# Optimization experiments

Hardware: AMD Instinct MI355X
Metric: run time of the kernel (lower is better)

## Reference

```python
import jax, jax.numpy as jnp
import numpy as np

B, T, V, D, H, HS, FF, L = 4, 1024, 32000, 1024, 16, 64, 4096, 8
STD = 0.02

def _ln(x, g, b, eps=1e-5):
    m = x.mean(-1, keepdims=True)
    v = ((x - m) ** 2).mean(-1, keepdims=True)
    return (x - m) / jnp.sqrt(v + eps) * g + b

def setup_inputs() -> dict:
    key = jax.random.key(0)
    ks = jax.random.split(key, 16)
    n = lambda k, shp: jax.random.normal(k, shp, dtype=jnp.float32) * STD
    inp = {
        "idx": jax.random.randint(ks[0], (B, T), 0, V),
        "tok_emb": n(ks[1], (V, D)),
        "pos_emb": n(ks[2], (T, D)),
        # per-layer stacked attention weights; [D, H, HS] per layer (no bias)
        "Wq": n(ks[3], (L, D, H, HS)),
        "Wk": n(ks[4], (L, D, H, HS)),
        "Wv": n(ks[5], (L, D, H, HS)),
        "Wp": n(ks[6], (L, H * HS, D)),
        "bp": jnp.zeros((L, D), jnp.float32),
        "ln1_g": jnp.ones((L, D), jnp.float32),
        "ln1_b": jnp.zeros((L, D), jnp.float32),
        "ln2_g": jnp.ones((L, D), jnp.float32),
        "ln2_b": jnp.zeros((L, D), jnp.float32),
        "W1": n(ks[7], (L, D, FF)),
        "b1": jnp.zeros((L, FF), jnp.float32),
        "W2": n(ks[8], (L, FF, D)),
        "b2": jnp.zeros((L, D), jnp.float32),
        "lnf_g": jnp.ones((D,), jnp.float32),
        "lnf_b": jnp.zeros((D,), jnp.float32),
        "Wlm": n(ks[9], (D, V)),
        "blm": jnp.zeros((V,), jnp.float32),
    }
    return inp

def reference(idx, tok_emb, pos_emb, Wq, Wk, Wv, Wp, bp, ln1_g, ln1_b,
              ln2_g, ln2_b, W1, b1, W2, b2, lnf_g, lnf_b, Wlm, blm):
    Bb, Tt = idx.shape
    x = tok_emb[idx] + pos_emb[:Tt]                      # [B,T,D]
    causal = jnp.tril(jnp.ones((Tt, Tt), bool))          # tril mask
    for l in range(L):
        xn = _ln(x, ln1_g[l], ln1_b[l])
        q = jnp.einsum('btd,dhk->bhtk', xn, Wq[l])
        k = jnp.einsum('btd,dhk->bhtk', xn, Wk[l])
        v = jnp.einsum('btd,dhk->bhtk', xn, Wv[l])
        w = jnp.einsum('bhtk,bhsk->bhts', q, k) * (HS ** -0.5)
        w = jnp.where(causal, w, -jnp.inf)
        w = jax.nn.softmax(w, axis=-1)
        o = jnp.einsum('bhts,bhsk->bhtk', w, v)
        o = o.transpose(0, 2, 1, 3).reshape(Bb, Tt, H * HS)  # concat heads
        x = x + o @ Wp[l] + bp[l]
        xn = _ln(x, ln2_g[l], ln2_b[l])
        x = x + jax.nn.relu(xn @ W1[l] + b1[l]) @ W2[l] + b2[l]
    x = _ln(x, lnf_g, lnf_b)
    logits = x @ Wlm + blm                               # [B,T,V]
    return logits
```

## Files before the change

### kernel.cpp

```cpp
#include <hip/hip_runtime.h>
#include <cstdint>

typedef __attribute__((ext_vector_type(4))) float f32x4;
typedef __attribute__((ext_vector_type(8))) short s16x8;
typedef __attribute__((ext_vector_type(4))) short s16x4;
typedef unsigned short u16;
typedef unsigned int u32;
typedef __attribute__((address_space(1))) void gas_void;
typedef __attribute__((address_space(3))) void las_void;

#define B_ 4
#define T_ 1024
#define V_ 32000
#define D_ 1024
#define H_ 16
#define HS_ 64
#define FF_ 4096
#define L_ 8
#define BT_ (B_ * T_)

__device__ __forceinline__ float bf2f(u16 h) { return __uint_as_float(((u32)h) << 16); }
__device__ __forceinline__ u16 f2bf(float f) {
  u32 u = __float_as_uint(f);
  u += 0x7fffu + ((u >> 16) & 1u);
  return (u16)(u >> 16);
}

__device__ __forceinline__ void gld16(const void* g, void* l) {
  __builtin_amdgcn_global_load_lds((gas_void*)(uintptr_t)g,
                                   (las_void*)(u32)(uintptr_t)l, 16, 0, 0);
}


template <int EPI>
__global__ __launch_bounds__(512, 2) void gemm256(
    const u16* __restrict__ A, const u16* __restrict__ Bt,
    const float* __restrict__ bias, float* Cf, u16* Cb,
    int M, int N, int K, int nrowb) {
  __shared__ u16 lds[2][2][2][8192];
  const int tid = threadIdx.x;
  const int lane = tid & 63;
  const int lr = lane & 15, hi = lane >> 4;
  const int wid = tid >> 6;
  const int wm128 = (wid >> 2) << 7;
  const int wn64 = (wid & 3) << 6;
  const int logical = ((int)blockIdx.x & 7) * ((int)gridDim.x >> 3) + ((int)blockIdx.x >> 3);
  const int row0 = (logical % nrowb) << 8;
  const int col0 = (logical / nrowb) << 8;
  const int NT = K >> 6;
  const int srow = tid >> 2;
  const int schunk = tid & 3;
  const int xo = ((hi + (lr >> 1)) & 3) << 4;

  f32x4 acc[32];
#pragma unroll
  for (int i = 0; i < 32; ++i) acc[i] = f32x4{0.f, 0.f, 0.f, 0.f};
  s16x8 bfr[4];

#define VMW(N) asm volatile("s_waitcnt vmcnt(" #N ")" ::: "memory")

#define STG(DB, DK, OP, KT)                                                    \
  {                                                                            \
    const u16* sp_ = (OP) ? Bt : A;                                            \
    const int base_ = (OP) ? col0 : row0;                                      \
    const int c0_ = ((KT) << 6) + ((DK) << 5);                                 \
    _Pragma("unroll")                                                          \
    for (int sh_ = 0; sh_ < 2; ++sh_) {                                        \
      const int rr_ = (sh_ << 7) + srow;                                       \
      const int ko_ = ((schunk - (rr_ >> 1)) & 3) << 3;                        \
      gld16(sp_ + (size_t)(base_ + rr_) * K + c0_ + ko_,                       \
            (char*)&lds[DB][DK][OP][0] + (sh_ << 13) + (wid << 10));           \
    }                                                                          \
  }

#define PHASE(BUF, MH, KS, LOADB, STG_STMT, VM_STMT)                           \
  {                                                                            \
    __builtin_amdgcn_sched_barrier(0);                                         \
    const char* As_ = (const char*)&lds[BUF][KS][0][0];                        \
    const char* Bs_ = (const char*)&lds[BUF][KS][1][0];                        \
    const int ra_ = wm128 + ((MH) << 6) + lr;                                  \
    s16x8 af_[4];                                                              \
    _Pragma("unroll")                                                          \
    for (int q_ = 0; q_ < 4; ++q_)                                             \
      af_[q_] = *(const s16x8*)(As_ + ((ra_ + (q_ << 4)) << 6) + xo);          \
    if (LOADB) {                                                               \
      _Pragma("unroll")                                                        \
      for (int q_ = 0; q_ < 4; ++q_)                                           \
        bfr[q_] = *(const s16x8*)(Bs_ + ((wn64 + lr + (q_ << 4)) << 6) + xo);  \
    }                                                                          \
    STG_STMT;                                                                  \
    __builtin_amdgcn_sched_barrier(0);                                         \
    __builtin_amdgcn_s_barrier();                                              \
    asm volatile("s_waitcnt lgkmcnt(0)" ::: "memory");                         \
    __builtin_amdgcn_sched_barrier(0);                                         \
    __builtin_amdgcn_s_setprio(1);                                             \
    _Pragma("unroll")                                                          \
    for (int mi_ = 0; mi_ < 4; ++mi_) {                                        \
      _Pragma("unroll")                                                        \
      for (int nj_ = 0; nj_ < 4; ++nj_)                                        \
        acc[((MH)*4 + mi_) * 4 + nj_] = __builtin_amdgcn_mfma_f32_16x16x32_bf16( \
            af_[mi_], bfr[nj_], acc[((MH)*4 + mi_) * 4 + nj_], 0, 0, 0);       \
    }                                                                          \
    __builtin_amdgcn_s_setprio(0);                                             \
    __builtin_amdgcn_sched_barrier(0);                                         \
    VM_STMT;                                                                   \
    __builtin_amdgcn_s_barrier();                                              \
  }

  STG(0, 0, 0, 0)
  STG(0, 0, 1, 0)
  STG(0, 1, 0, 0)
  STG(0, 1, 1, 0)
  STG(1, 0, 0, 1)
  STG(1, 0, 1, 1)
  VMW(8);
  __builtin_amdgcn_s_barrier();

  const int NI = NT >> 1;
  for (int it = 0; it < NI - 1; ++it) {
    const int t1 = 2 * it + 1, t2 = 2 * it + 2, t3 = 2 * it + 3;
    PHASE(0, 0, 0, 1, STG(1, 1, 0, t1), )
    PHASE(0, 1, 0, 0, STG(1, 1, 1, t1), VMW(6))
    PHASE(0, 0, 1, 1, STG(0, 0, 0, t2), )
    PHASE(0, 1, 1, 0, STG(0, 0, 1, t2), VMW(6))
    PHASE(1, 0, 0, 1, STG(0, 1, 0, t2), )
    PHASE(1, 1, 0, 0, STG(0, 1, 1, t2), VMW(6))
    PHASE(1, 0, 1, 1, STG(1, 0, 0, t3), )
    PHASE(1, 1, 1, 0, STG(1, 0, 1, t3), VMW(6))
  }
  {
    PHASE(0, 0, 0, 1, STG(1, 1, 0, NT - 1), )
    PHASE(0, 1, 0, 0, STG(1, 1, 1, NT - 1), VMW(8))
    PHASE(0, 0, 1, 1, (void)0, )
    PHASE(0, 1, 1, 0, (void)0, VMW(4))
    PHASE(1, 0, 0, 1, (void)0, )
    PHASE(1, 1, 0, 0, (void)0, VMW(0))
    PHASE(1, 0, 1, 1, (void)0, )
    PHASE(1, 1, 1, 0, (void)0, )
  }
#undef PHASE
#undef STG
#undef VMW

  const int gr0 = row0 + wm128;
  const int gc0 = col0 + wn64;
#pragma unroll
  for (int nj = 0; nj < 4; ++nj) {
    const int col = gc0 + (nj << 4) + lr;
    const float bv = (EPI != 0) ? bias[col] : 0.f;
#pragma unroll
    for (int mi = 0; mi < 8; ++mi) {
#pragma unroll
      for (int rg = 0; rg < 4; ++rg) {
        const int row = gr0 + (mi << 4) + (hi << 2) + rg;
        const size_t off = (size_t)row * N + col;
        float val = acc[mi * 4 + nj][rg] + bv;
        if constexpr (EPI == 2) val = fmaxf(val, 0.f);
        if constexpr (EPI == 0 || EPI == 2) Cb[off] = f2bf(val);
        else Cf[off] = val;
      }
    }
  }
}

template <int EPI>
__global__ __launch_bounds__(256) void gemm_bt(
    const u16* __restrict__ A, const u16* __restrict__ Bt,
    const float* __restrict__ bias, float* Cf, u16* Cb,
    int M, int N, int K) {
  __shared__ u16 lds[2][2][4096];
  const int tid = threadIdx.x;
  const int lane = tid & 63;
  const int lr = lane & 15, hi = lane >> 4;
  const int wid = tid >> 6;
  const int wm = wid >> 1, wn = wid & 1;
  const int row0 = blockIdx.y << 7, col0 = blockIdx.x << 7;
  const int NT = K >> 5;
  const int wbase = (tid & ~63) << 4;
  const int xo = ((hi + (lr >> 1)) & 3) << 4;

  f32x4 acc[4][4];
#pragma unroll
  for (int i = 0; i < 4; ++i)
#pragma unroll
    for (int j = 0; j < 4; ++j) acc[i][j] = f32x4{0.f, 0.f, 0.f, 0.f};

  auto stage = [&](int buf, int kt) {
#pragma unroll
    for (int c = 0; c < 2; ++c) {
      const int o = (c << 12) + (tid << 4);
      const int r = o >> 6;
      const int ko = ((((o >> 4) & 3) - (r >> 1)) & 3) << 3;
      gld16(A + (size_t)(row0 + r) * K + (kt << 5) + ko,
            (char*)&lds[buf][0][0] + (c << 12) + wbase);
      gld16(Bt + (size_t)(col0 + r) * K + (kt << 5) + ko,
            (char*)&lds[buf][1][0] + (c << 12) + wbase);
    }
  };

  stage(0, 0);
  __syncthreads();
  int cur = 0;
  for (int kt = 0; kt < NT; ++kt) {
    if (kt + 1 < NT) stage(cur ^ 1, kt + 1);
    const char* As = (const char*)&lds[cur][0][0];
    const char* Bs = (const char*)&lds[cur][1][0];
    s16x8 af[4], bfr[4];
#pragma unroll
    for (int i = 0; i < 4; ++i) {
      const int ra = (wm << 6) + (i << 4) + lr;
      af[i] = *(const s16x8*)(As + (ra << 6) + xo);
      const int rb = (wn << 6) + (i << 4) + lr;
      bfr[i] = *(const s16x8*)(Bs + (rb << 6) + xo);
    }
#pragma unroll
    for (int i = 0; i < 4; ++i)
#pragma unroll
      for (int j = 0; j < 4; ++j)
        acc[i][j] =
            __builtin_amdgcn_mfma_f32_16x16x32_bf16(af[i], bfr[j], acc[i][j], 0, 0, 0);
    __syncthreads();
    cur ^= 1;
  }

  const int gr = row0 + (wm << 6);
  const int gc = col0 + (wn << 6);
#pragma unroll
  for (int j = 0; j < 4; ++j) {
    const int col = gc + (j << 4) + lr;
    const float bv = (EPI != 0) ? bias[col] : 0.f;
#pragma unroll
    for (int i = 0; i < 4; ++i) {
#pragma unroll
      for (int rg = 0; rg < 4; ++rg) {
        const int row = gr + (i << 4) + (hi << 2) + rg;
        const size_t off = (size_t)row * N + col;
        float val = acc[i][j][rg] + bv;
        if constexpr (EPI == 1) val += Cf[off];
        if constexpr (EPI == 2) val = fmaxf(val, 0.f);
        if constexpr (EPI == 0 || EPI == 2) Cb[off] = f2bf(val);
        else Cf[off] = val;
      }
    }
  }
}

__global__ __launch_bounds__(256) void ln_kernel(const float* __restrict__ x,
                                                 const float* __restrict__ gw,
                                                 const float* __restrict__ bw,
                                                 u16* __restrict__ out) {
  const int r = blockIdx.x, tid = threadIdx.x;
  const int lane = tid & 63, wid = tid >> 6;
  __shared__ float red[8];
  f32x4 v = *(const f32x4*)(x + ((size_t)r << 10) + (tid << 2));
  float s = v[0] + v[1] + v[2] + v[3];
  float q = v[0] * v[0] + v[1] * v[1] + v[2] * v[2] + v[3] * v[3];
#pragma unroll
  for (int off = 32; off; off >>= 1) {
    s += __shfl_down(s, off);
    q += __shfl_down(q, off);
  }
  if (lane == 0) {
    red[wid] = s;
    red[4 + wid] = q;
  }
  __syncthreads();
  const float mean = (red[0] + red[1] + red[2] + red[3]) * (1.f / 1024.f);
  const float var = (red[4] + red[5] + red[6] + red[7]) * (1.f / 1024.f) - mean * mean;
  const float rstd = rsqrtf(var + 1e-5f);
  f32x4 g4 = *(const f32x4*)(gw + (tid << 2));
  f32x4 b4 = *(const f32x4*)(bw + (tid << 2));
  u16* op = out + ((size_t)r << 10) + (tid << 2);
#pragma unroll
  for (int j = 0; j < 4; ++j) op[j] = f2bf((v[j] - mean) * rstd * g4[j] + b4[j]);
}

__global__ __launch_bounds__(256) void embed_kernel(const int* __restrict__ idx,
                                                    const float* __restrict__ tok,
                                                    const float* __restrict__ pos,
                                                    float* __restrict__ x) {
  const int r = blockIdx.x, tid = threadIdx.x;
  const int t = r & (T_ - 1);
  const int tk = idx[r];
  f32x4 a = *(const f32x4*)(tok + ((size_t)tk << 10) + (tid << 2));
  f32x4 p = *(const f32x4*)(pos + ((size_t)t << 10) + (tid << 2));
  *(f32x4*)(x + ((size_t)r << 10) + (tid << 2)) = a + p;
}

__global__ __launch_bounds__(256) void tconv_kernel(const float* __restrict__ src,
                                                    u16* __restrict__ dst, int K, int N) {
  __shared__ float tile[32][33];
  const int tx = threadIdx.x & 31, ty = threadIdx.x >> 5;
  const int n0 = blockIdx.x << 5, k0 = blockIdx.y << 5;
#pragma unroll
  for (int i = 0; i < 32; i += 8)
    tile[ty + i][tx] = src[(size_t)(k0 + ty + i) * N + n0 + tx];
  __syncthreads();
#pragma unroll
  for (int i = 0; i < 32; i += 8)
    dst[(size_t)(n0 + ty + i) * K + k0 + tx] = f2bf(tile[tx][ty + i]);
}

__global__ __launch_bounds__(256) void fattn_kernel(const u16* __restrict__ qkv,
                                                    u16* __restrict__ o) {
  const int qt = blockIdx.x, h = blockIdx.y, b = blockIdx.z;
  const int tid = threadIdx.x;
  const int lane = tid & 63;
  const int lr = lane & 15, hi = lane >> 4;
  const int w = tid >> 6;
  __shared__ alignas(16) u16 Kl[2][4096];
  __shared__ alignas(16) u16 Vt[2][4096];

  const size_t bT = (size_t)(b * T_);
  const int q_row = (qt << 6) + (w << 4) + lr;
  const size_t qbase = (bT + q_row) * 3072 + (h << 6);
  s16x8 aq[2];
  aq[0] = *(const s16x8*)(qkv + qbase + hi * 8);
  aq[1] = *(const s16x8*)(qkv + qbase + 32 + hi * 8);

  f32x4 ofr[4];
#pragma unroll
  for (int j = 0; j < 4; ++j) ofr[j] = f32x4{0.f, 0.f, 0.f, 0.f};
  float mrun = -1e30f, lsum = 0.f;

  uint4 vr0, vr1;

#define STAGEK(BUF, KT)                                                        \
  {                                                                            \
    _Pragma("unroll")                                                          \
    for (int sh_ = 0; sh_ < 2; ++sh_) {                                        \
      const int ob_ = (sh_ << 12) + (tid << 4);                                \
      const int r_ = ob_ >> 7;                                                 \
      const int il_ = (ob_ & 127) ^ ((r_ & 7) << 4);                           \
      gld16(qkv + (bT + ((KT) << 6) + r_) * 3072 + 1024 + (h << 6) + (il_ >> 1), \
            (char*)&Kl[BUF][0] + (sh_ << 12) + ((tid & 192) << 4));            \
    }                                                                          \
  }
#define LOADV(KT)                                                              \
  {                                                                            \
    const u16* vs_ =                                                           \
        qkv + (bT + ((KT) << 6) + lane) * 3072 + 2048 + (h << 6) + (w << 4);   \
    vr0 = *(const uint4*)vs_;                                                  \
    vr1 = *(const uint4*)(vs_ + 8);                                            \
  }
#define WRITEV(BUF)                                                            \
  {                                                                            \
    const u16* p0_ = (const u16*)&vr0;                                         \
    const u16* p1_ = (const u16*)&vr1;                                         \
    _Pragma("unroll")                                                          \
    for (int j_ = 0; j_ < 8; ++j_) {                                           \
      const int sw_ = lane ^ (j_ << 3);                                        \
      Vt[BUF][(((w << 4) + j_) << 6) + sw_] = p0_[j_];                         \
      Vt[BUF][(((w << 4) + 8 + j_) << 6) + sw_] = p1_[j_];                     \
    }                                                                          \
  }

  STAGEK(0, 0)
  LOADV(0)
  asm volatile("s_waitcnt vmcnt(0)" ::: "memory");
  WRITEV(0)
  asm volatile("s_waitcnt lgkmcnt(0)" ::: "memory");
  __builtin_amdgcn_sched_barrier(0);
  __builtin_amdgcn_s_barrier();

  int cur = 0;
  for (int kt = 0; kt <= qt; ++kt) {
    if (kt < qt) {
      STAGEK(cur ^ 1, kt + 1)
      LOADV(kt + 1)
    }

    f32x4 s[4];
#pragma unroll
    for (int j = 0; j < 4; ++j) s[j] = f32x4{0.f, 0.f, 0.f, 0.f};
    __builtin_amdgcn_s_setprio(1);
#pragma unroll
    for (int kk = 0; kk < 2; ++kk)
#pragma unroll
      for (int j = 0; j < 4; ++j) {
        const int rb = (j << 4) + lr;
        const s16x8 bk = *(const s16x8*)((const char*)&Kl[cur][0] + (rb << 7) +
                                         ((((kk << 2) + hi) ^ (rb & 7)) << 4));
        s[j] = __builtin_amdgcn_mfma_f32_16x16x32_bf16(bk, aq[kk], s[j], 0, 0, 0);
      }
    __builtin_amdgcn_s_setprio(0);

    if (kt == qt) {
      const int qr = (w << 4) + lr;
#pragma unroll
      for (int j = 0; j < 4; ++j)
#pragma unroll
        for (int rg = 0; rg < 4; ++rg) {
          const int kvr = (j << 4) + (hi << 2) + rg;
          s[j][rg] = (kvr > qr) ? -1e30f : s[j][rg] * 0.125f;
        }
    } else {
#pragma unroll
      for (int j = 0; j < 4; ++j) s[j] = s[j] * 0.125f;
    }

    float mx = -1e30f;
#pragma unroll
    for (int j = 0; j < 4; ++j)
#pragma unroll
      for (int rg = 0; rg < 4; ++rg) mx = fmaxf(mx, s[j][rg]);
    mx = fmaxf(mx, __shfl_xor(mx, 16));
    mx = fmaxf(mx, __shfl_xor(mx, 32));
    const float mn = fmaxf(mrun, mx);
    const float sc = __expf(mrun - mn);
    mrun = mn;
    float rs = 0.f;
#pragma unroll
    for (int j = 0; j < 4; ++j)
#pragma unroll
      for (int rg = 0; rg < 4; ++rg) {
        const float e = __expf(s[j][rg] - mn);
        s[j][rg] = e;
        rs += e;
      }
    rs += __shfl_xor(rs, 16);
    rs += __shfl_xor(rs, 32);
    lsum = lsum * sc + rs;
    float scO[4];
#pragma unroll
    for (int rg = 0; rg < 4; ++rg) scO[rg] = __shfl(sc, (hi << 2) + rg);
#pragma unroll
    for (int j2 = 0; j2 < 4; ++j2)
#pragma unroll
      for (int rg = 0; rg < 4; ++rg) ofr[j2][rg] *= scO[rg];

    s16x8 pb[2];
#pragma unroll
    for (int kk = 0; kk < 2; ++kk)
#pragma unroll
      for (int i = 0; i < 4; ++i) {
        pb[kk][i] = (short)f2bf(s[2 * kk][i]);
        pb[kk][4 + i] = (short)f2bf(s[2 * kk + 1][i]);
      }

    __builtin_amdgcn_s_setprio(1);
#pragma unroll
    for (int kk = 0; kk < 2; ++kk)
#pragma unroll
      for (int j2 = 0; j2 < 4; ++j2) {
        const int drow = (j2 << 4) + lr;
        const int swz = (drow & 7) << 3;
        const int base = drow << 6;
        const s16x4 lo = *(const s16x4*)&Vt[cur][base + (((kk << 5) + (hi << 2)) ^ swz)];
        const s16x4 hv = *(const s16x4*)&Vt[cur][base + (((kk << 5) + 16 + (hi << 2)) ^ swz)];
        const s16x8 vb = __builtin_shufflevector(lo, hv, 0, 1, 2, 3, 4, 5, 6, 7);
        ofr[j2] = __builtin_amdgcn_mfma_f32_16x16x32_bf16(pb[kk], vb, ofr[j2], 0, 0, 0);
      }
    __builtin_amdgcn_s_setprio(0);

    if (kt < qt) {
      asm volatile("s_waitcnt vmcnt(0)" ::: "memory");
      WRITEV(cur ^ 1)
    }
    asm volatile("s_waitcnt lgkmcnt(0)" ::: "memory");
    __builtin_amdgcn_sched_barrier(0);
    __builtin_amdgcn_s_barrier();
    cur ^= 1;
  }

  const float rinv = 1.f / lsum;
  float rO[4];
#pragma unroll
  for (int rg = 0; rg < 4; ++rg) rO[rg] = __shfl(rinv, (hi << 2) + rg);
#pragma unroll
  for (int j2 = 0; j2 < 4; ++j2)
#pragma unroll
    for (int rg = 0; rg < 4; ++rg) {
      const int row = (qt << 6) + (w << 4) + (hi << 2) + rg;
      const int col = (h << 6) + (j2 << 4) + lr;
      o[(bT + row) * 1024 + col] = f2bf(ofr[j2][rg] * rO[rg]);
    }
#undef STAGEK
#undef LOADV
#undef WRITEV
}

extern "C" void kernel_launch(void* const* d_in, const int* in_sizes, int n_in,
                              void* d_out, int out_size, void* d_ws, size_t ws_size,
                              hipStream_t stream) {
  (void)in_sizes; (void)n_in; (void)out_size; (void)ws_size;
  const int* idx = (const int*)d_in[0];
  const float* tokE = (const float*)d_in[1];
  const float* posE = (const float*)d_in[2];
  const float* Wq = (const float*)d_in[3];
  const float* Wk = (const float*)d_in[4];
  const float* Wv = (const float*)d_in[5];
  const float* Wp = (const float*)d_in[6];
  const float* bp = (const float*)d_in[7];
  const float* ln1g = (const float*)d_in[8];
  const float* ln1b = (const float*)d_in[9];
  const float* ln2g = (const float*)d_in[10];
  const float* ln2b = (const float*)d_in[11];
  const float* W1 = (const float*)d_in[12];
  const float* b1 = (const float*)d_in[13];
  const float* W2 = (const float*)d_in[14];
  const float* b2 = (const float*)d_in[15];
  const float* lnfg = (const float*)d_in[16];
  const float* lnfb = (const float*)d_in[17];
  const float* Wlm = (const float*)d_in[18];
  const float* blm = (const float*)d_in[19];

  char* p = (char*)d_ws;
  float* x = (float*)p;   p += (size_t)BT_ * D_ * 4;
  u16* xn = (u16*)p;      p += (size_t)BT_ * D_ * 2;
  u16* qkv = (u16*)p;     p += (size_t)BT_ * 3072 * 2;
  u16* ob = (u16*)p;      p += (size_t)BT_ * D_ * 2;
  u16* hb = (u16*)p;      p += (size_t)BT_ * FF_ * 2;
  u16* WqkvT = (u16*)p;   p += (size_t)L_ * 3072 * D_ * 2;
  u16* WpT = (u16*)p;     p += (size_t)L_ * D_ * D_ * 2;
  u16* W1T = (u16*)p;     p += (size_t)L_ * FF_ * D_ * 2;
  u16* W2T = (u16*)p;     p += (size_t)L_ * D_ * FF_ * 2;
  u16* WlmT = (u16*)p;    p += (size_t)V_ * D_ * 2;

  dim3 blk(256);
  dim3 blk512(512);
  for (int l = 0; l < L_; ++l) {
    tconv_kernel<<<dim3(32, 32), blk, 0, stream>>>(Wq + (size_t)l * D_ * D_,
                                                   WqkvT + (size_t)l * 3072 * D_, D_, D_);
    tconv_kernel<<<dim3(32, 32), blk, 0, stream>>>(
        Wk + (size_t)l * D_ * D_, WqkvT + (size_t)l * 3072 * D_ + D_ * D_, D_, D_);
    tconv_kernel<<<dim3(32, 32), blk, 0, stream>>>(
        Wv + (size_t)l * D_ * D_, WqkvT + (size_t)l * 3072 * D_ + 2 * D_ * D_, D_, D_);
    tconv_kernel<<<dim3(32, 32), blk, 0, stream>>>(Wp + (size_t)l * D_ * D_,
                                                   WpT + (size_t)l * D_ * D_, D_, D_);
    tconv_kernel<<<dim3(128, 32), blk, 0, stream>>>(W1 + (size_t)l * D_ * FF_,
                                                    W1T + (size_t)l * FF_ * D_, D_, FF_);
    tconv_kernel<<<dim3(32, 128), blk, 0, stream>>>(W2 + (size_t)l * FF_ * D_,
                                                    W2T + (size_t)l * D_ * FF_, FF_, D_);
  }
  tconv_kernel<<<dim3(1000, 32), blk, 0, stream>>>(Wlm, WlmT, D_, V_);

  embed_kernel<<<dim3(BT_), blk, 0, stream>>>(idx, tokE, posE, x);

  for (int l = 0; l < L_; ++l) {
    ln_kernel<<<dim3(BT_), blk, 0, stream>>>(x, ln1g + l * D_, ln1b + l * D_, xn);
    gemm_bt<0><<<dim3(24, 32), blk, 0, stream>>>(xn, WqkvT + (size_t)l * 3072 * D_,
                                                 nullptr, nullptr, qkv, BT_, 3072, D_);
    fattn_kernel<<<dim3(T_ / 64, H_, B_), blk, 0, stream>>>(qkv, ob);
    gemm_bt<1><<<dim3(8, 32), blk, 0, stream>>>(ob, WpT + (size_t)l * D_ * D_,
                                                bp + l * D_, x, nullptr, BT_, D_, D_);
    ln_kernel<<<dim3(BT_), blk, 0, stream>>>(x, ln2g + l * D_, ln2b + l * D_, xn);
    gemm256<2><<<dim3(256), blk512, 0, stream>>>(xn, W1T + (size_t)l * FF_ * D_,
                                                 b1 + l * FF_, nullptr, hb, BT_, FF_, D_, 16);
    gemm_bt<1><<<dim3(8, 32), blk, 0, stream>>>(hb, W2T + (size_t)l * D_ * FF_,
                                                b2 + l * D_, x, nullptr, BT_, D_, FF_);
  }
  ln_kernel<<<dim3(BT_), blk, 0, stream>>>(x, lnfg, lnfb, xn);
  gemm256<3><<<dim3(2000), blk512, 0, stream>>>(xn, WlmT, blm, (float*)d_out, nullptr,
                                                BT_, V_, D_, 16);
}
```

Measured before the change: 2.967 ms.

## Batch weight transposes, use wave-per-row layernorm, remap attention blocks across XCDs

The per-layer weight transpose launches are merged into three batched launches that select the layer and matrix from blockIdx.z. LayerNorm now gives each 64-lane wave a whole row, reducing with xor shuffles instead of shared memory and a barrier, and writes bf16 output as 4-element vectors. The flash-attention block index is remapped so blocks sharing a (batch, head) pair land on the same XCD, aiming for better L2 reuse of K/V. Together these cut launch count, sync overhead and cache misses at the cost of more complex indexing.

```diff
diff --git a/kernel.cpp b/kernel.cpp
--- a/kernel.cpp
+++ b/kernel.cpp
@@ -249,30 +249,39 @@
                                                  const float* __restrict__ gw,
                                                  const float* __restrict__ bw,
                                                  u16* __restrict__ out) {
-  const int r = blockIdx.x, tid = threadIdx.x;
-  const int lane = tid & 63, wid = tid >> 6;
-  __shared__ float red[8];
-  f32x4 v = *(const f32x4*)(x + ((size_t)r << 10) + (tid << 2));
-  float s = v[0] + v[1] + v[2] + v[3];
-  float q = v[0] * v[0] + v[1] * v[1] + v[2] * v[2] + v[3] * v[3];
+  const int lane = threadIdx.x & 63;
+  const size_t r = ((size_t)blockIdx.x << 2) + (threadIdx.x >> 6);
+  const float* xp = x + (r << 10);
+  f32x4 v[4];
+  float s = 0.f, q = 0.f;
+#pragma unroll
+  for (int j = 0; j < 4; ++j) {
+    v[j] = *(const f32x4*)(xp + (lane << 2) + (j << 8));
+#pragma unroll
+    for (int e = 0; e < 4; ++e) {
+      s += v[j][e];
+      q += v[j][e] * v[j][e];
+    }
+  }
 #pragma unroll
   for (int off = 32; off; off >>= 1) {
-    s += __shfl_down(s, off);
-    q += __shfl_down(q, off);
-  }
-  if (lane == 0) {
-    red[wid] = s;
-    red[4 + wid] = q;
-  }
-  __syncthreads();
-  const float mean = (red[0] + red[1] + red[2] + red[3]) * (1.f / 1024.f);
-  const float var = (red[4] + red[5] + red[6] + red[7]) * (1.f / 1024.f) - mean * mean;
+    s += __shfl_xor(s, off);
+    q += __shfl_xor(q, off);
+  }
+  const float mean = s * (1.f / 1024.f);
+  const float var = q * (1.f / 1024.f) - mean * mean;
   const float rstd = rsqrtf(var + 1e-5f);
-  f32x4 g4 = *(const f32x4*)(gw + (tid << 2));
-  f32x4 b4 = *(const f32x4*)(bw + (tid << 2));
-  u16* op = out + ((size_t)r << 10) + (tid << 2);
-#pragma unroll
-  for (int j = 0; j < 4; ++j) op[j] = f2bf((v[j] - mean) * rstd * g4[j] + b4[j]);
+  u16* op = out + (r << 10);
+#pragma unroll
+  for (int j = 0; j < 4; ++j) {
+    const f32x4 g4 = *(const f32x4*)(gw + (lane << 2) + (j << 8));
+    const f32x4 b4 = *(const f32x4*)(bw + (lane << 2) + (j << 8));
+    s16x4 o4;
+#pragma unroll
+    for (int e = 0; e < 4; ++e)
+      o4[e] = (short)f2bf((v[j][e] - mean) * rstd * g4[e] + b4[e]);
+    *(s16x4*)(op + (lane << 2) + (j << 8)) = o4;
+  }
 }
 
 __global__ __launch_bounds__(256) void embed_kernel(const int* __restrict__ idx,
@@ -287,23 +296,59 @@
   *(f32x4*)(x + ((size_t)r << 10) + (tid << 2)) = a + p;
 }
 
+#define TCONV_BODY(SRC, DST, KK, NN)                                           \
+  {                                                                            \
+    __shared__ float tile[32][33];                                             \
+    const int tx = threadIdx.x & 31, ty = threadIdx.x >> 5;                    \
+    const int n0 = blockIdx.x << 5, k0 = blockIdx.y << 5;                      \
+    _Pragma("unroll")                                                          \
+    for (int i = 0; i < 32; i += 8)                                            \
+      tile[ty + i][tx] = (SRC)[(size_t)(k0 + ty + i) * (NN) + n0 + tx];        \
+    __syncthreads();                                                           \
+    _Pragma("unroll")                                                          \
+    for (int i = 0; i < 32; i += 8)                                            \
+      (DST)[(size_t)(n0 + ty + i) * (KK) + k0 + tx] = f2bf(tile[tx][ty + i]);  \
+  }
+
+__global__ __launch_bounds__(256) void tconv_qkvp(
+    const float* __restrict__ Wq, const float* __restrict__ Wk,
+    const float* __restrict__ Wv, const float* __restrict__ Wp,
+    u16* __restrict__ WqkvT, u16* __restrict__ WpT) {
+  const int z = blockIdx.z;
+  const int l = z >> 2, m = z & 3;
+  const float* src;
+  u16* dst;
+  if (m == 0) { src = Wq + (size_t)l * D_ * D_; dst = WqkvT + (size_t)l * 3072 * D_; }
+  else if (m == 1) { src = Wk + (size_t)l * D_ * D_; dst = WqkvT + (size_t)l * 3072 * D_ + D_ * D_; }
+  else if (m == 2) { src = Wv + (size_t)l * D_ * D_; dst = WqkvT + (size_t)l * 3072 * D_ + 2 * D_ * D_; }
+  else { src = Wp + (size_t)l * D_ * D_; dst = WpT + (size_t)l * D_ * D_; }
+  TCONV_BODY(src, dst, D_, D_)
+}
+
+__global__ __launch_bounds__(256) void tconv_w1(const float* __restrict__ W1,
+                                                u16* __restrict__ W1T) {
+  const int l = blockIdx.z;
+  TCONV_BODY(W1 + (size_t)l * D_ * FF_, W1T + (size_t)l * FF_ * D_, D_, FF_)
+}
+
+__global__ __launch_bounds__(256) void tconv_w2(const float* __restrict__ W2,
+                                                u16* __restrict__ W2T) {
+  const int l = blockIdx.z;
+  TCONV_BODY(W2 + (size_t)l * FF_ * D_, W2T + (size_t)l * D_ * FF_, FF_, D_)
+}
+
 __global__ __launch_bounds__(256) void tconv_kernel(const float* __restrict__ src,
                                                     u16* __restrict__ dst, int K, int N) {
-  __shared__ float tile[32][33];
-  const int tx = threadIdx.x & 31, ty = threadIdx.x >> 5;
-  const int n0 = blockIdx.x << 5, k0 = blockIdx.y << 5;
-#pragma unroll
-  for (int i = 0; i < 32; i += 8)
-    tile[ty + i][tx] = src[(size_t)(k0 + ty + i) * N + n0 + tx];
-  __syncthreads();
-#pragma unroll
-  for (int i = 0; i < 32; i += 8)
-    dst[(size_t)(n0 + ty + i) * K + k0 + tx] = f2bf(tile[tx][ty + i]);
+  TCONV_BODY(src, dst, K, N)
 }
 
 __global__ __launch_bounds__(256) void fattn_kernel(const u16* __restrict__ qkv,
                                                     u16* __restrict__ o) {
-  const int qt = blockIdx.x, h = blockIdx.y, b = blockIdx.z;
+  const int flat = (int)blockIdx.x + ((int)blockIdx.y << 4) + ((int)blockIdx.z << 8);
+  const int xcd = flat & 7, seq = flat >> 3;
+  const int pair = (xcd << 3) + (seq >> 4);
+  const int qt = seq & 15;
+  const int h = pair & 15, b = pair >> 4;
   const int tid = threadIdx.x;
   const int lane = tid & 63;
   const int lr = lane & 15, hi = lane >> 4;
@@ -519,38 +564,27 @@
 
   dim3 blk(256);
   dim3 blk512(512);
+  tconv_qkvp<<<dim3(32, 32, 32), blk, 0, stream>>>(Wq, Wk, Wv, Wp, WqkvT, WpT);
+  tconv_w1<<<dim3(128, 32, 8), blk, 0, stream>>>(W1, W1T);
+  tconv_w2<<<dim3(32, 128, 8), blk, 0, stream>>>(W2, W2T);
+  tconv_kernel<<<dim3(1000, 32), blk, 0, stream>>>(Wlm, WlmT, D_, V_);
+
+  embed_kernel<<<dim3(BT_), blk, 0, stream>>>(idx, tokE, posE, x);
+
   for (int l = 0; l < L_; ++l) {
-    tconv_kernel<<<dim3(32, 32), blk, 0, stream>>>(Wq + (size_t)l * D_ * D_,
-                                                   WqkvT + (size_t)l * 3072 * D_, D_, D_);
-    tconv_kernel<<<dim3(32, 32), blk, 0, stream>>>(
-        Wk + (size_t)l * D_ * D_, WqkvT + (size_t)l * 3072 * D_ + D_ * D_, D_, D_);
-    tconv_kernel<<<dim3(32, 32), blk, 0, stream>>>(
-        Wv + (size_t)l * D_ * D_, WqkvT + (size_t)l * 3072 * D_ + 2 * D_ * D_, D_, D_);
-    tconv_kernel<<<dim3(32, 32), blk, 0, stream>>>(Wp + (size_t)l * D_ * D_,
-                                                   WpT + (size_t)l * D_ * D_, D_, D_);
-    tconv_kernel<<<dim3(128, 32), blk, 0, stream>>>(W1 + (size_t)l * D_ * FF_,
-                                                    W1T + (size_t)l * FF_ * D_, D_, FF_);
-    tconv_kernel<<<dim3(32, 128), blk, 0, stream>>>(W2 + (size_t)l * FF_ * D_,
-                                                    W2T + (size_t)l * D_ * FF_, FF_, D_);
-  }
-  tconv_kernel<<<dim3(1000, 32), blk, 0, stream>>>(Wlm, WlmT, D_, V_);
-
-  embed_kernel<<<dim3(BT_), blk, 0, stream>>>(idx, tokE, posE, x);
-
-  for (int l = 0; l < L_; ++l) {
-    ln_kernel<<<dim3(BT_), blk, 0, stream>>>(x, ln1g + l * D_, ln1b + l * D_, xn);
+    ln_kernel<<<dim3(BT_ / 4), blk, 0, stream>>>(x, ln1g + l * D_, ln1b + l * D_, xn);
     gemm_bt<0><<<dim3(24, 32), blk, 0, stream>>>(xn, WqkvT + (size_t)l * 3072 * D_,
                                                  nullptr, nullptr, qkv, BT_, 3072, D_);
     fattn_kernel<<<dim3(T_ / 64, H_, B_), blk, 0, stream>>>(qkv, ob);
     gemm_bt<1><<<dim3(8, 32), blk, 0, stream>>>(ob, WpT + (size_t)l * D_ * D_,
                                                 bp + l * D_, x, nullptr, BT_, D_, D_);
-    ln_kernel<<<dim3(BT_), blk, 0, stream>>>(x, ln2g + l * D_, ln2b + l * D_, xn);
+    ln_kernel<<<dim3(BT_ / 4), blk, 0, stream>>>(x, ln2g + l * D_, ln2b + l * D_, xn);
     gemm256<2><<<dim3(256), blk512, 0, stream>>>(xn, W1T + (size_t)l * FF_ * D_,
                                                  b1 + l * FF_, nullptr, hb, BT_, FF_, D_, 16);
     gemm_bt<1><<<dim3(8, 32), blk, 0, stream>>>(hb, W2T + (size_t)l * D_ * FF_,
                                                 b2 + l * D_, x, nullptr, BT_, D_, FF_);
   }
-  ln_kernel<<<dim3(BT_), blk, 0, stream>>>(x, lnfg, lnfb, xn);
+  ln_kernel<<<dim3(BT_ / 4), blk, 0, stream>>>(x, lnfg, lnfb, xn);
   gemm256<3><<<dim3(2000), blk512, 0, stream>>>(xn, WlmT, blm, (float*)d_out, nullptr,
                                                 BT_, V_, D_, 16);
 }
```

After: 2.707 ms. -8.8%, faster.
